# Kernel optimization log

Hardware: AMD Instinct MI355X
Metric: run time of the kernel (lower is better)

The kernel has to match this reference:

```python
import jax, jax.numpy as jnp
import numpy as np

DIM = 1024
HEADS = 16
DIM_HEAD = 64
INNER = HEADS * DIM_HEAD  # 1024
FEAT = 1024  # cfg.different_learnable_tokens=False -> feature_dim = dim
EPS = 1e-5
SCALE = 1.0 / np.sqrt(DIM_HEAD)


def setup_inputs() -> dict:
    key = jax.random.key(0)
    ks = jax.random.split(key, 10)
    b, n = 2, 2048
    x = jax.random.normal(ks[0], (b, n, DIM), jnp.float32)
    y = jax.random.normal(ks[1], (b, n, FEAT), jnp.float32)
    # learned parameters
    ln_g = jnp.ones((DIM,), jnp.float32)
    ln_b = jnp.zeros((DIM,), jnp.float32)
    w_qkv = jax.random.normal(ks[2], (DIM, 3 * INNER), jnp.float32) * (DIM ** -0.5)
    w_av = jax.random.normal(ks[3], (FEAT, INNER), jnp.float32) * (FEAT ** -0.5)
    w_out = jax.random.normal(ks[4], (INNER, DIM), jnp.float32) * (INNER ** -0.5)
    b_out = jnp.zeros((DIM,), jnp.float32)
    w_yout = jax.random.normal(ks[5], (INNER, FEAT), jnp.float32) * (INNER ** -0.5)
    b_yout = jnp.zeros((FEAT,), jnp.float32)
    return {"x": x, "y": y, "ln_g": ln_g, "ln_b": ln_b, "w_qkv": w_qkv,
            "w_av": w_av, "w_out": w_out, "b_out": b_out,
            "w_yout": w_yout, "b_yout": b_yout}


def _split_heads(t):  # [b,n,(h d)] -> [b,h,n,d]
    b, n, _ = t.shape
    return t.reshape(b, n, HEADS, DIM_HEAD).transpose(0, 2, 1, 3)


def _merge_heads(t):  # [b,h,n,d] -> [b,n,(h d)]
    b, h, n, d = t.shape
    return t.transpose(0, 2, 1, 3).reshape(b, n, h * d)


def reference(x, y, ln_g, ln_b, w_qkv, w_av, w_out, b_out, w_yout, b_yout):
    # LayerNorm
    mu = jnp.mean(x, axis=-1, keepdims=True)
    var = jnp.mean(jnp.square(x - mu), axis=-1, keepdims=True)
    xn = (x - mu) * jax.lax.rsqrt(var + EPS) * ln_g + ln_b

    qkv = xn @ w_qkv  # [b,n,3*inner]
    q, k, v = jnp.split(qkv, 3, axis=-1)
    av = y @ w_av  # [b,n,inner]
    q, k, v, av = map(_split_heads, (q, k, v, av))  # [b,h,n,d]

    # shared QK softmax, applied to both V and another_v
    scores = jnp.einsum('bhnd,bhmd->bhnm', q, k) * SCALE
    attn = jax.nn.softmax(scores, axis=-1)
    x_ctx = jnp.einsum('bhnm,bhmd->bhnd', attn, v)
    y_ctx = jnp.einsum('bhnm,bhmd->bhnd', attn, av)

    x_out = _merge_heads(x_ctx) @ w_out + b_out
    y_out = _merge_heads(y_ctx) @ w_yout + b_yout
    return (x_out, y_out)
```

## Files before the change

### kernel.cpp

```cpp
#include <hip/hip_runtime.h>

typedef _Float16 half8 __attribute__((ext_vector_type(8)));
typedef _Float16 half4v __attribute__((ext_vector_type(4)));
typedef float f32x4 __attribute__((ext_vector_type(4)));
typedef unsigned int u32;

#define SEQ 2048
#define NTOK 4096
#define DM 1024
#define QKS 2048
#define LN_EPS 1e-5f
#define LOG2E_SCALE 0.18033688f

typedef const __attribute__((address_space(1))) u32* gas_ptr;
typedef __attribute__((address_space(3))) u32* las_ptr;
__device__ __forceinline__ void gld_lds16(const void* g, void* l) {
  __builtin_amdgcn_global_load_lds((gas_ptr)g, (las_ptr)l, 16, 0, 0);
}

#define BARRIER() do { __builtin_amdgcn_s_barrier(); __builtin_amdgcn_sched_barrier(0); } while (0)
#define VMW(N) do { asm volatile("s_waitcnt vmcnt(" #N ")" ::: "memory"); __builtin_amdgcn_sched_barrier(0); } while (0)
#define LGW() do { asm volatile("s_waitcnt lgkmcnt(0)" ::: "memory"); __builtin_amdgcn_sched_barrier(0); } while (0)

__global__ __launch_bounds__(256) void prep_kernel(
    const float* __restrict__ x, const float* __restrict__ g, const float* __restrict__ bta,
    const float* __restrict__ y,
    const float* __restrict__ w_qkv, const float* __restrict__ w_av,
    const float* __restrict__ w_out, const float* __restrict__ w_yout,
    _Float16* __restrict__ xn, _Float16* __restrict__ yh,
    _Float16* __restrict__ wqkvT, _Float16* __restrict__ wavT,
    _Float16* __restrict__ woutT, _Float16* __restrict__ wyoutT) {
  __shared__ float smem[64 * 65];
  const int bid = blockIdx.x;
  const int t = threadIdx.x;
  if (bid < 4096) {
    const int row = bid;
    const float4 v = ((const float4*)(x + (size_t)row * DM))[t];
    float s = v.x + v.y + v.z + v.w;
#pragma unroll
    for (int m = 1; m < 64; m <<= 1) s += __shfl_xor(s, m, 64);
    float* red = smem;
    const int wid = t >> 6, lane = t & 63;
    if (lane == 0) red[wid] = s;
    __syncthreads();
    const float mu = (red[0] + red[1] + red[2] + red[3]) * (1.0f / DM);
    const float dx = v.x - mu, dy = v.y - mu, dz = v.z - mu, dw = v.w - mu;
    float ss = dx * dx + dy * dy + dz * dz + dw * dw;
#pragma unroll
    for (int m = 1; m < 64; m <<= 1) ss += __shfl_xor(ss, m, 64);
    __syncthreads();
    if (lane == 0) red[wid] = ss;
    __syncthreads();
    const float var = (red[0] + red[1] + red[2] + red[3]) * (1.0f / DM);
    const float rstd = rsqrtf(var + LN_EPS);
    const float4 gg = ((const float4*)g)[t];
    const float4 bb = ((const float4*)bta)[t];
    half4v o;
    o[0] = (_Float16)(dx * rstd * gg.x + bb.x);
    o[1] = (_Float16)(dy * rstd * gg.y + bb.y);
    o[2] = (_Float16)(dz * rstd * gg.z + bb.z);
    o[3] = (_Float16)(dw * rstd * gg.w + bb.w);
    *(half4v*)(xn + (size_t)row * DM + t * 4) = o;
  } else if (bid < 8192) {
    const int row = bid - 4096;
    const float4 v = ((const float4*)(y + (size_t)row * DM))[t];
    half4v o;
    o[0] = (_Float16)v.x; o[1] = (_Float16)v.y;
    o[2] = (_Float16)v.z; o[3] = (_Float16)v.w;
    *(half4v*)(yh + (size_t)row * DM + t * 4) = o;
  } else {
    const int id2 = bid - 8192;
    const float* W; _Float16* WT; int Nc, bx, by;
    if (id2 < 768) { W = w_qkv; WT = wqkvT; Nc = 3072; bx = id2 % 48; by = id2 / 48; }
    else {
      const int id3 = id2 - 768, sel = id3 >> 8;
      Nc = 1024; bx = id3 & 15; by = (id3 >> 4) & 15;
      if (sel == 0) { W = w_av; WT = wavT; }
      else if (sel == 1) { W = w_out; WT = woutT; }
      else { W = w_yout; WT = wyoutT; }
    }
    float (*tile)[65] = (float(*)[65])smem;
    const int n0 = bx * 64, k0 = by * 64;
    const int c = t & 63;
#pragma unroll
    for (int i = 0; i < 16; i++) {
      const int r = (t >> 6) * 16 + i;
      tile[r][c] = W[(size_t)(k0 + r) * Nc + n0 + c];
    }
    __syncthreads();
#pragma unroll
    for (int i = 0; i < 16; i++) {
      const int n = (t >> 6) * 16 + i;
      WT[(size_t)(n0 + n) * 1024 + k0 + c] = (_Float16)tile[c][n];
    }
  }
}

__global__ __launch_bounds__(512, 2) void gemm8p_kernel(
    const _Float16* __restrict__ xn, const _Float16* __restrict__ wqkvT,
    const _Float16* __restrict__ yh, const _Float16* __restrict__ wavT,
    _Float16* __restrict__ qkvm, _Float16* __restrict__ vtb,
    _Float16* __restrict__ avtb) {
  __shared__ _Float16 Ab[2][8192];
  __shared__ _Float16 Bb[2][8192];
  const int swz = ((blockIdx.x & 7) << 5) + (blockIdx.x >> 3);
  const _Float16 *A, *B;
  int m0, n0, isav;
  if (swz < 192) { A = xn; B = wqkvT; m0 = (swz / 12) * 256; n0 = (swz % 12) * 256; isav = 0; }
  else { const int u = swz - 192; A = yh; B = wavT; m0 = (u >> 2) * 256; n0 = (u & 3) * 256; isav = 1; }
  const int t = threadIdx.x;
  const int wid = t >> 6, lane = t & 63, lo = lane & 15, hi = lane >> 4;
  const int wm = wid >> 2, wn = wid & 3;
  const int srow = t >> 2;
  const int sx = ((t & 3) ^ (srow & 3)) << 3;
  const _Float16* gA = A + (size_t)(m0 + srow) * 1024 + sx;
  const _Float16* gB = B + (size_t)(n0 + srow) * 1024 + sx;
  const int rdz = (hi ^ (lo & 3)) << 3;
  const int arow = (wm * 128 + lo) * 32 + rdz;
  const int brow = (wn * 64 + lo) * 32 + rdz;

  f32x4 acc[8][4];
#pragma unroll
  for (int i = 0; i < 8; i++)
#pragma unroll
    for (int j = 0; j < 4; j++) {
      acc[i][j][0] = 0.f; acc[i][j][1] = 0.f; acc[i][j][2] = 0.f; acc[i][j][3] = 0.f;
    }
  half8 af[4], bf[4];

#define STG_A(BUF, HH, KT) gld_lds16(gA + (HH) * 131072 + (KT) * 32, &Ab[BUF][(HH) * 4096 + t * 8])
#define STG_B(BUF, HH, KT) gld_lds16(gB + (HH) * 131072 + (KT) * 32, &Bb[BUF][(HH) * 4096 + t * 8])
#define RDA(BUF, FB)                                                     \
  _Pragma("unroll") for (int f2 = 0; f2 < 4; f2++)                       \
      af[f2] = *(const half8*)&Ab[BUF][arow + ((FB) + f2) * 512]
#define RDB(BUF, G0)                                                     \
  _Pragma("unroll") for (int g2 = 0; g2 < 2; g2++)                       \
      bf[(G0) + g2] = *(const half8*)&Bb[BUF][brow + ((G0) + g2) * 512]
#define MMA(FB, G0)                                                      \
  do {                                                                   \
    __builtin_amdgcn_s_setprio(1);                                       \
    _Pragma("unroll") for (int f2 = 0; f2 < 4; f2++)                     \
        _Pragma("unroll") for (int g2 = 0; g2 < 2; g2++)                 \
            acc[(FB) + f2][(G0) + g2] = __builtin_amdgcn_mfma_f32_16x16x32_f16( \
                af[f2], bf[(G0) + g2], acc[(FB) + f2][(G0) + g2], 0, 0, 0); \
    __builtin_amdgcn_s_setprio(0);                                       \
  } while (0)

  STG_A(0, 0, 0); STG_A(0, 1, 0); STG_B(0, 0, 0); STG_B(0, 1, 0);
  STG_A(1, 0, 1);

  for (int it = 0; it < 16; it++) {
    const int T1 = 2 * it + 1;
    const int N0 = (2 * it + 2) & 31, N1 = (2 * it + 3) & 31;
    VMW(1); BARRIER();
    RDA(0, 0); RDB(0, 0);
    STG_A(1, 1, T1);
    LGW(); MMA(0, 0);
    BARRIER(); RDB(0, 2); STG_B(1, 0, T1); LGW(); MMA(0, 2);
    BARRIER(); RDA(0, 4); STG_B(1, 1, T1); LGW(); MMA(4, 2);
    BARRIER(); STG_A(0, 0, N0); MMA(4, 0);
    VMW(1); BARRIER();
    RDA(1, 0); RDB(1, 0);
    STG_A(0, 1, N0);
    LGW(); MMA(0, 0);
    BARRIER(); RDB(1, 2); STG_B(0, 0, N0); LGW(); MMA(0, 2);
    BARRIER(); RDA(1, 4); STG_B(0, 1, N0); LGW(); MMA(4, 2);
    BARRIER(); STG_A(1, 0, N1); MMA(4, 0);
  }
#undef STG_A
#undef STG_B
#undef RDA
#undef RDB
#undef MMA

#pragma unroll
  for (int f = 0; f < 8; f++)
#pragma unroll
    for (int g = 0; g < 4; g++)
#pragma unroll
      for (int r = 0; r < 4; r++) {
        const int row = m0 + wm * 128 + f * 16 + 4 * hi + r;
        const int col = n0 + wn * 64 + g * 16 + lo;
        const _Float16 v = (_Float16)acc[f][g][r];
        if (!isav && col < 2048) {
          qkvm[(size_t)row * QKS + col] = v;
        } else {
          const int coff = isav ? col : col - 2048;
          _Float16* Ct = isav ? avtb : vtb;
          Ct[(((size_t)((row >> 11) << 4) + (coff >> 6)) * 64 + (coff & 63)) * SEQ +
             (row & (SEQ - 1))] = v;
        }
      }
}

__global__ __launch_bounds__(256) void gemmout_kernel(
    const _Float16* __restrict__ A0, const _Float16* __restrict__ B0,
    float* F0, const float* bias0, int nblk0,
    const _Float16* __restrict__ A1, const _Float16* __restrict__ B1,
    float* F1, const float* bias1) {
  __shared__ _Float16 As[128 * 32];
  __shared__ _Float16 Bs[128 * 32];
  int id = ((blockIdx.x & 7) * (gridDim.x >> 3)) + (blockIdx.x >> 3);
  const _Float16 *A, *BT;
  float* Cf; const float* bias;
  if (id < nblk0) { A = A0; BT = B0; Cf = F0; bias = bias0; }
  else { id -= nblk0; A = A1; BT = B1; Cf = F1; bias = bias1; }
  const int bx = id & 7, by = id >> 3;
  const int t = threadIdx.x;
  const int wid = t >> 6, lane = t & 63, lo = lane & 15, hi = lane >> 4;
  const int wm = wid >> 1, wn = wid & 1;
  const int m0 = by * 128, n0 = bx * 128;
  const int K = 1024;

  f32x4 acc[4][4];
#pragma unroll
  for (int i = 0; i < 4; i++)
#pragma unroll
    for (int j = 0; j < 4; j++) {
      acc[i][j][0] = 0.f; acc[i][j][1] = 0.f; acc[i][j][2] = 0.f; acc[i][j][3] = 0.f;
    }
  const int rowA = t >> 2;
  const int kcol = (t & 3) * 8;
  const _Float16* gA = A + (size_t)(m0 + rowA) * K + kcol;
  const _Float16* gB = BT + (size_t)(n0 + rowA) * K + kcol;

  for (int k0 = 0; k0 < K; k0 += 32) {
#pragma unroll
    for (int j = 0; j < 2; j++) {
      gld_lds16(gA + (size_t)(j * 64) * K + k0, As + j * 2048 + wid * 512);
      gld_lds16(gB + (size_t)(j * 64) * K + k0, Bs + j * 2048 + wid * 512);
    }
    __syncthreads();
    half8 af[4], bf[4];
#pragma unroll
    for (int i = 0; i < 4; i++) {
      af[i] = *(const half8*)(As + (wm * 64 + i * 16 + lo) * 32 + hi * 8);
      bf[i] = *(const half8*)(Bs + (wn * 64 + i * 16 + lo) * 32 + hi * 8);
    }
#pragma unroll
    for (int i = 0; i < 4; i++)
#pragma unroll
      for (int j = 0; j < 4; j++)
        acc[i][j] = __builtin_amdgcn_mfma_f32_16x16x32_f16(af[i], bf[j], acc[i][j], 0, 0, 0);
    __syncthreads();
  }
#pragma unroll
  for (int i = 0; i < 4; i++)
#pragma unroll
    for (int j = 0; j < 4; j++)
#pragma unroll
      for (int r = 0; r < 4; r++) {
        const int row = m0 + wm * 64 + i * 16 + 4 * hi + r;
        const int col = n0 + wn * 64 + j * 16 + lo;
        Cf[(size_t)row * 1024 + col] = acc[i][j][r] + bias[col];
      }
}

__global__ __launch_bounds__(256) void attn_kernel(
    const _Float16* __restrict__ qkvm,
    const _Float16* __restrict__ vt,
    const _Float16* __restrict__ avt,
    _Float16* __restrict__ xctx, _Float16* __restrict__ yctx) {
  __shared__ _Float16 Kl[2][4096];
  __shared__ _Float16 Vl[4096];
  __shared__ _Float16 Al[4096];
  __shared__ _Float16 Pl[4][2048];

  const int t = threadIdx.x;
  const int wid = t >> 6, lane = t & 63, lo = lane & 15, hi = lane >> 4;
  const int l7 = lane & 7;
  const int id = blockIdx.x;
  const int bh = ((id & 7) << 2) + ((id >> 3) >> 4);
  const int qt = (id >> 3) & 15;
  const int b = bh >> 4, h = bh & 15;
  const int q0 = qt * 128 + wid * 32;
  const size_t tokbase = (size_t)b * SEQ;
  const _Float16* vbase = vt + (size_t)bh * 64 * SEQ;
  const _Float16* abase = avt + (size_t)bh * 64 * SEQ;
  _Float16* Pw = Pl[wid];
  const int NT = SEQ / 64;

  half8 qf[2][2];
#pragma unroll
  for (int rg = 0; rg < 2; rg++)
#pragma unroll
    for (int kc = 0; kc < 2; kc++)
      qf[rg][kc] = *(const half8*)(qkvm + (tokbase + q0 + rg * 16 + lo) * QKS +
                                   h * 64 + kc * 32 + hi * 8);

  f32x4 zero;
  zero[0] = 0.f; zero[1] = 0.f; zero[2] = 0.f; zero[3] = 0.f;
  f32x4 accx[2][4], accy[2][4];
  float mC[2], lsum[2];
#pragma unroll
  for (int rg = 0; rg < 2; rg++) {
#pragma unroll
    for (int j = 0; j < 4; j++) { accx[rg][j] = zero; accy[rg][j] = zero; }
    mC[rg] = -1.0e30f; lsum[rg] = 0.0f;
  }

  const int skey = t >> 3;
  const int sc7 = t & 7;

#define STAGE_K(kv0, BSEL)                                                        \
  do {                                                                            \
    _Pragma("unroll") for (int j = 0; j < 2; j++) {                               \
      const int key = skey + j * 32;                                              \
      const int cs = ((sc7 ^ (key & 7)) << 3);                                    \
      gld_lds16(qkvm + (tokbase + (kv0) + key) * QKS + DM + h * 64 + cs,          \
                &Kl[BSEL][j * 2048 + wid * 512]);                                 \
    }                                                                             \
  } while (0)

#define STAGE_VA(kv0)                                                             \
  do {                                                                            \
    _Pragma("unroll") for (int j = 0; j < 2; j++) {                               \
      const int drow = skey + j * 32;                                             \
      const int cs = ((sc7 ^ (drow & 7)) << 3);                                   \
      gld_lds16(vbase + (size_t)drow * SEQ + (kv0) + cs,                          \
                &Vl[j * 2048 + wid * 512]);                                       \
      gld_lds16(abase + (size_t)drow * SEQ + (kv0) + cs,                          \
                &Al[j * 2048 + wid * 512]);                                       \
    }                                                                             \
  } while (0)

  STAGE_K(0, 0);
  STAGE_VA(0);
  STAGE_K(64, 1);

  for (int tt = 0; tt < NT; tt++) {
    if (tt + 2 < NT) { VMW(2); } else { VMW(0); }
    BARRIER();
    const _Float16* Kb = Kl[tt & 1];

    f32x4 s[2][4];
#pragma unroll
    for (int kg = 0; kg < 4; kg++) {
      const int kr = (kg * 16 + lo) * 64;
      const half8 ak0 = *(const half8*)(Kb + kr + ((hi ^ l7) << 3));
      const half8 ak1 = *(const half8*)(Kb + kr + (((4 | hi) ^ l7) << 3));
#pragma unroll
      for (int rg = 0; rg < 2; rg++) {
        f32x4 z = __builtin_amdgcn_mfma_f32_16x16x32_f16(ak0, qf[rg][0], zero, 0, 0, 0);
        s[rg][kg] = __builtin_amdgcn_mfma_f32_16x16x32_f16(ak1, qf[rg][1], z, 0, 0, 0);
      }
    }

    float tmC[2];
#pragma unroll
    for (int rg = 0; rg < 2; rg++) {
      float tm = -3.0e38f;
#pragma unroll
      for (int kg = 0; kg < 4; kg++)
#pragma unroll
        for (int r = 0; r < 4; r++) tm = fmaxf(tm, s[rg][kg][r]);
      tm = fmaxf(tm, __shfl_xor(tm, 16, 64));
      tm = fmaxf(tm, __shfl_xor(tm, 32, 64));
      tmC[rg] = tm * LOG2E_SCALE;
    }

    const bool grow = (tmC[0] > mC[0] + 8.0f) | (tmC[1] > mC[1] + 8.0f);
    if (__any(grow)) {
      float fcs[2];
#pragma unroll
      for (int rg = 0; rg < 2; rg++) {
        const float mn = fmaxf(mC[rg], tmC[rg]);
        fcs[rg] = exp2f(mC[rg] - mn);
        mC[rg] = mn;
        lsum[rg] *= fcs[rg];
      }
#pragma unroll
      for (int rg = 0; rg < 2; rg++)
#pragma unroll
        for (int r = 0; r < 4; r++) {
          const float fcb = __shfl(fcs[rg], 4 * hi + r, 64);
#pragma unroll
          for (int ng = 0; ng < 4; ng++) {
            accx[rg][ng][r] *= fcb;
            accy[rg][ng][r] *= fcb;
          }
        }
    }

#pragma unroll
    for (int rg = 0; rg < 2; rg++) {
      float rs = 0.0f;
#pragma unroll
      for (int kg = 0; kg < 4; kg++) {
        half4v pk;
#pragma unroll
        for (int r = 0; r < 4; r++) {
          const float p = exp2f(fmaf(s[rg][kg][r], LOG2E_SCALE, -mC[rg]));
          rs += p;
          pk[r] = (_Float16)p;
        }
        *(half4v*)(Pw + (rg * 16 + lo) * 64 +
                   (((kg * 2 + (hi >> 1)) ^ l7) << 3) + ((hi & 1) << 2)) = pk;
      }
      rs += __shfl_xor(rs, 16, 64);
      rs += __shfl_xor(rs, 32, 64);
      lsum[rg] += rs;
    }

#pragma unroll
    for (int kk = 0; kk < 2; kk++) {
      half8 pa[2];
#pragma unroll
      for (int rg = 0; rg < 2; rg++)
        pa[rg] = *(const half8*)(Pw + (rg * 16 + lo) * 64 + (((kk * 4 + hi) ^ l7) << 3));
#pragma unroll
      for (int ng = 0; ng < 4; ng++) {
        const int vr = (ng * 16 + lo) * 64 + (((kk * 4 + hi) ^ l7) << 3);
        const half8 bv = *(const half8*)(Vl + vr);
        const half8 ba = *(const half8*)(Al + vr);
#pragma unroll
        for (int rg = 0; rg < 2; rg++) {
          accx[rg][ng] = __builtin_amdgcn_mfma_f32_16x16x32_f16(pa[rg], bv, accx[rg][ng], 0, 0, 0);
          accy[rg][ng] = __builtin_amdgcn_mfma_f32_16x16x32_f16(pa[rg], ba, accy[rg][ng], 0, 0, 0);
        }
      }
    }

    BARRIER();
    if (tt + 1 < NT) STAGE_VA((tt + 1) * 64);
    if (tt + 2 < NT) STAGE_K((tt + 2) * 64, tt & 1);
  }
#undef STAGE_K
#undef STAGE_VA

#pragma unroll
  for (int rg = 0; rg < 2; rg++) {
    const float inv = 1.0f / lsum[rg];
#pragma unroll
    for (int r = 0; r < 4; r++) {
      const float invb = __shfl(inv, 4 * hi + r, 64);
      const size_t tok = tokbase + q0 + rg * 16 + 4 * hi + r;
#pragma unroll
      for (int ng = 0; ng < 4; ng++) {
        const int col = h * 64 + ng * 16 + lo;
        xctx[tok * DM + col] = (_Float16)(accx[rg][ng][r] * invb);
        yctx[tok * DM + col] = (_Float16)(accy[rg][ng][r] * invb);
      }
    }
  }
}

extern "C" void kernel_launch(void* const* d_in, const int* in_sizes, int n_in,
                              void* d_out, int out_size, void* d_ws, size_t ws_size,
                              hipStream_t stream) {
  const float* x      = (const float*)d_in[0];
  const float* y      = (const float*)d_in[1];
  const float* ln_g   = (const float*)d_in[2];
  const float* ln_b   = (const float*)d_in[3];
  const float* w_qkv  = (const float*)d_in[4];
  const float* w_av   = (const float*)d_in[5];
  const float* w_out  = (const float*)d_in[6];
  const float* b_out  = (const float*)d_in[7];
  const float* w_yout = (const float*)d_in[8];
  const float* b_yout = (const float*)d_in[9];
  float* out = (float*)d_out;

  _Float16* ws     = (_Float16*)d_ws;
  _Float16* xn     = ws;
  _Float16* yh     = xn + 4194304;
  _Float16* wqkvT  = yh + 4194304;
  _Float16* wavT   = wqkvT + 3145728;
  _Float16* woutT  = wavT + 1048576;
  _Float16* wyoutT = woutT + 1048576;
  _Float16* qkvm   = wyoutT + 1048576;
  _Float16* vtb    = qkvm + 8388608;
  _Float16* avtb   = vtb + 4194304;
  _Float16* xc     = avtb + 4194304;
  _Float16* yc     = xc + 4194304;

  prep_kernel<<<9728, 256, 0, stream>>>(x, ln_g, ln_b, y, w_qkv, w_av, w_out, w_yout,
                                        xn, yh, wqkvT, wavT, woutT, wyoutT);

  gemm8p_kernel<<<256, 512, 0, stream>>>(xn, wqkvT, yh, wavT, qkvm, vtb, avtb);

  attn_kernel<<<512, 256, 0, stream>>>(qkvm, vtb, avtb, xc, yc);

  gemmout_kernel<<<512, 256, 0, stream>>>(
      xc, woutT, out, b_out, 256,
      yc, wyoutT, out + 4194304, b_yout);
}
```

Baseline: 238.3 us.

## Use 256x256 double-buffered output GEMM and register-staged V/AV prefetch in attention

The output projection GEMM moves from a 128x128 single-buffer kernel on 512 blocks to a 256x256-tile kernel with 512 threads, double-buffered swizzled LDS, interleaved staging and MFMA phases, and setprio around the MFMA groups, launched on 128 blocks. This aims to raise data reuse per tile and overlap global loads with compute. The attention kernel now prefetches V/AV tiles into registers one step ahead and writes them to LDS after compute, while K is staged one tile ahead instead of two. This changes the wait-count schedule. The trade-off is fewer blocks than CUs for the GEMM (possible underutilisation), higher register pressure, and more complex synchronisation.

Result: no change. 242.1 us (+1.6%).

```diff
diff --git a/kernel.cpp b/kernel.cpp
--- a/kernel.cpp
+++ b/kernel.cpp
@@ -193,66 +193,94 @@
       }
 }
 
-__global__ __launch_bounds__(256) void gemmout_kernel(
-    const _Float16* __restrict__ A0, const _Float16* __restrict__ B0,
-    float* F0, const float* bias0, int nblk0,
-    const _Float16* __restrict__ A1, const _Float16* __restrict__ B1,
-    float* F1, const float* bias1) {
-  __shared__ _Float16 As[128 * 32];
-  __shared__ _Float16 Bs[128 * 32];
-  int id = ((blockIdx.x & 7) * (gridDim.x >> 3)) + (blockIdx.x >> 3);
-  const _Float16 *A, *BT;
-  float* Cf; const float* bias;
-  if (id < nblk0) { A = A0; BT = B0; Cf = F0; bias = bias0; }
-  else { id -= nblk0; A = A1; BT = B1; Cf = F1; bias = bias1; }
-  const int bx = id & 7, by = id >> 3;
+__global__ __launch_bounds__(512, 2) void gemmout8p_kernel(
+    const _Float16* __restrict__ xc, const _Float16* __restrict__ woutT,
+    float* __restrict__ o0, const float* __restrict__ b0,
+    const _Float16* __restrict__ yc, const _Float16* __restrict__ wyoutT,
+    float* __restrict__ o1, const float* __restrict__ b1) {
+  __shared__ _Float16 Ab[2][8192];
+  __shared__ _Float16 Bb[2][8192];
+  const int swz = ((blockIdx.x & 7) << 4) + (blockIdx.x >> 3);
+  const _Float16 *A, *B;
+  float* F; const float* bias;
+  int u;
+  if (swz < 64) { A = xc; B = woutT; F = o0; bias = b0; u = swz; }
+  else { A = yc; B = wyoutT; F = o1; bias = b1; u = swz - 64; }
+  const int m0 = (u >> 2) * 256, n0 = (u & 3) * 256;
   const int t = threadIdx.x;
   const int wid = t >> 6, lane = t & 63, lo = lane & 15, hi = lane >> 4;
-  const int wm = wid >> 1, wn = wid & 1;
-  const int m0 = by * 128, n0 = bx * 128;
-  const int K = 1024;
-
-  f32x4 acc[4][4];
-#pragma unroll
-  for (int i = 0; i < 4; i++)
+  const int wm = wid >> 2, wn = wid & 3;
+  const int srow = t >> 2;
+  const int sx = ((t & 3) ^ (srow & 3)) << 3;
+  const _Float16* gA = A + (size_t)(m0 + srow) * 1024 + sx;
+  const _Float16* gB = B + (size_t)(n0 + srow) * 1024 + sx;
+  const int rdz = (hi ^ (lo & 3)) << 3;
+  const int arow = (wm * 128 + lo) * 32 + rdz;
+  const int brow = (wn * 64 + lo) * 32 + rdz;
+
+  f32x4 acc[8][4];
+#pragma unroll
+  for (int i = 0; i < 8; i++)
 #pragma unroll
     for (int j = 0; j < 4; j++) {
       acc[i][j][0] = 0.f; acc[i][j][1] = 0.f; acc[i][j][2] = 0.f; acc[i][j][3] = 0.f;
     }
-  const int rowA = t >> 2;
-  const int kcol = (t & 3) * 8;
-  const _Float16* gA = A + (size_t)(m0 + rowA) * K + kcol;
-  const _Float16* gB = BT + (size_t)(n0 + rowA) * K + kcol;
-
-  for (int k0 = 0; k0 < K; k0 += 32) {
-#pragma unroll
-    for (int j = 0; j < 2; j++) {
-      gld_lds16(gA + (size_t)(j * 64) * K + k0, As + j * 2048 + wid * 512);
-      gld_lds16(gB + (size_t)(j * 64) * K + k0, Bs + j * 2048 + wid * 512);
-    }
-    __syncthreads();
-    half8 af[4], bf[4];
-#pragma unroll
-    for (int i = 0; i < 4; i++) {
-      af[i] = *(const half8*)(As + (wm * 64 + i * 16 + lo) * 32 + hi * 8);
-      bf[i] = *(const half8*)(Bs + (wn * 64 + i * 16 + lo) * 32 + hi * 8);
-    }
-#pragma unroll
-    for (int i = 0; i < 4; i++)
-#pragma unroll
-      for (int j = 0; j < 4; j++)
-        acc[i][j] = __builtin_amdgcn_mfma_f32_16x16x32_f16(af[i], bf[j], acc[i][j], 0, 0, 0);
-    __syncthreads();
-  }
-#pragma unroll
-  for (int i = 0; i < 4; i++)
-#pragma unroll
-    for (int j = 0; j < 4; j++)
+  half8 af[4], bf[4];
+
+#define STG_A(BUF, HH, KT) gld_lds16(gA + (HH) * 131072 + (KT) * 32, &Ab[BUF][(HH) * 4096 + t * 8])
+#define STG_B(BUF, HH, KT) gld_lds16(gB + (HH) * 131072 + (KT) * 32, &Bb[BUF][(HH) * 4096 + t * 8])
+#define RDA(BUF, FB)                                                     \
+  _Pragma("unroll") for (int f2 = 0; f2 < 4; f2++)                       \
+      af[f2] = *(const half8*)&Ab[BUF][arow + ((FB) + f2) * 512]
+#define RDB(BUF, G0)                                                     \
+  _Pragma("unroll") for (int g2 = 0; g2 < 2; g2++)                       \
+      bf[(G0) + g2] = *(const half8*)&Bb[BUF][brow + ((G0) + g2) * 512]
+#define MMA(FB, G0)                                                      \
+  do {                                                                   \
+    __builtin_amdgcn_s_setprio(1);                                       \
+    _Pragma("unroll") for (int f2 = 0; f2 < 4; f2++)                     \
+        _Pragma("unroll") for (int g2 = 0; g2 < 2; g2++)                 \
+            acc[(FB) + f2][(G0) + g2] = __builtin_amdgcn_mfma_f32_16x16x32_f16( \
+                af[f2], bf[(G0) + g2], acc[(FB) + f2][(G0) + g2], 0, 0, 0); \
+    __builtin_amdgcn_s_setprio(0);                                       \
+  } while (0)
+
+  STG_A(0, 0, 0); STG_A(0, 1, 0); STG_B(0, 0, 0); STG_B(0, 1, 0);
+  STG_A(1, 0, 1);
+
+  for (int it = 0; it < 16; it++) {
+    const int T1 = 2 * it + 1;
+    const int N0 = (2 * it + 2) & 31, N1 = (2 * it + 3) & 31;
+    VMW(1); BARRIER();
+    RDA(0, 0); RDB(0, 0);
+    STG_A(1, 1, T1);
+    LGW(); MMA(0, 0);
+    BARRIER(); RDB(0, 2); STG_B(1, 0, T1); LGW(); MMA(0, 2);
+    BARRIER(); RDA(0, 4); STG_B(1, 1, T1); LGW(); MMA(4, 2);
+    BARRIER(); STG_A(0, 0, N0); MMA(4, 0);
+    VMW(1); BARRIER();
+    RDA(1, 0); RDB(1, 0);
+    STG_A(0, 1, N0);
+    LGW(); MMA(0, 0);
+    BARRIER(); RDB(1, 2); STG_B(0, 0, N0); LGW(); MMA(0, 2);
+    BARRIER(); RDA(1, 4); STG_B(0, 1, N0); LGW(); MMA(4, 2);
+    BARRIER(); STG_A(1, 0, N1); MMA(4, 0);
+  }
+#undef STG_A
+#undef STG_B
+#undef RDA
+#undef RDB
+#undef MMA
+
+#pragma unroll
+  for (int f = 0; f < 8; f++)
+#pragma unroll
+    for (int g = 0; g < 4; g++)
 #pragma unroll
       for (int r = 0; r < 4; r++) {
-        const int row = m0 + wm * 64 + i * 16 + 4 * hi + r;
-        const int col = n0 + wn * 64 + j * 16 + lo;
-        Cf[(size_t)row * 1024 + col] = acc[i][j][r] + bias[col];
+        const int row = m0 + wm * 128 + f * 16 + 4 * hi + r;
+        const int col = n0 + wn * 64 + g * 16 + lo;
+        F[(size_t)row * 1024 + col] = acc[f][g][r] + bias[col];
       }
 }
 
@@ -312,25 +340,39 @@
     }                                                                             \
   } while (0)
 
-#define STAGE_VA(kv0)                                                             \
+  half8 vreg[2], areg[2];
+#define LOAD_VA(kv0)                                                              \
   do {                                                                            \
     _Pragma("unroll") for (int j = 0; j < 2; j++) {                               \
       const int drow = skey + j * 32;                                             \
       const int cs = ((sc7 ^ (drow & 7)) << 3);                                   \
-      gld_lds16(vbase + (size_t)drow * SEQ + (kv0) + cs,                          \
-                &Vl[j * 2048 + wid * 512]);                                       \
-      gld_lds16(abase + (size_t)drow * SEQ + (kv0) + cs,                          \
-                &Al[j * 2048 + wid * 512]);                                       \
+      vreg[j] = *(const half8*)(vbase + (size_t)drow * SEQ + (kv0) + cs);         \
+      areg[j] = *(const half8*)(abase + (size_t)drow * SEQ + (kv0) + cs);         \
     }                                                                             \
   } while (0)
 
+#define WRITE_VA()                                                                \
+  do {                                                                            \
+    _Pragma("unroll") for (int j = 0; j < 2; j++) {                               \
+      *(half8*)(Vl + j * 2048 + t * 8) = vreg[j];                                 \
+      *(half8*)(Al + j * 2048 + t * 8) = areg[j];                                 \
+    }                                                                             \
+  } while (0)
+
   STAGE_K(0, 0);
-  STAGE_VA(0);
-  STAGE_K(64, 1);
+#pragma unroll
+  for (int j = 0; j < 2; j++) {
+    const int drow = skey + j * 32;
+    const int cs = ((sc7 ^ (drow & 7)) << 3);
+    gld_lds16(vbase + (size_t)drow * SEQ + cs, &Vl[j * 2048 + wid * 512]);
+    gld_lds16(abase + (size_t)drow * SEQ + cs, &Al[j * 2048 + wid * 512]);
+  }
+  LOAD_VA(64);
 
   for (int tt = 0; tt < NT; tt++) {
-    if (tt + 2 < NT) { VMW(2); } else { VMW(0); }
+    if (tt + 1 < NT) { VMW(4); } else { VMW(0); }
     BARRIER();
+    if (tt + 1 < NT) STAGE_K((tt + 1) * 64, (tt & 1) ^ 1);
     const _Float16* Kb = Kl[tt & 1];
 
     f32x4 s[2][4];
@@ -421,12 +463,17 @@
       }
     }
 
-    BARRIER();
-    if (tt + 1 < NT) STAGE_VA((tt + 1) * 64);
-    if (tt + 2 < NT) STAGE_K((tt + 2) * 64, tt & 1);
+    if (tt + 1 < NT) {
+      VMW(2);
+      BARRIER();
+      WRITE_VA();
+      LGW();
+      if (tt + 2 < NT) LOAD_VA((tt + 2) * 64);
+    }
   }
 #undef STAGE_K
-#undef STAGE_VA
+#undef LOAD_VA
+#undef WRITE_VA
 
 #pragma unroll
   for (int rg = 0; rg < 2; rg++) {
@@ -480,7 +527,7 @@
 
   attn_kernel<<<512, 256, 0, stream>>>(qkvm, vtb, avtb, xc, yc);
 
-  gemmout_kernel<<<512, 256, 0, stream>>>(
-      xc, woutT, out, b_out, 256,
+  gemmout8p_kernel<<<128, 512, 0, stream>>>(
+      xc, woutT, out, b_out,
       yc, wyoutT, out + 4194304, b_yout);
 }
```
